# Performance work log

Measured on AMD Instinct MI355X. Metric: run time of the kernel, lower is better.

## Reference

```python
import jax, jax.numpy as jnp
import numpy as np

K = 128          # fixed max number of points per persistence diagram
BIG = 1e9        # sentinel for masked sort


def _extrema_masks(img):
    # 4-neighborhood local minima / maxima of a 2D image (boundary neighbors = +/-inf)
    p = jnp.pad(img, 1, constant_values=BIG)
    nmin = jnp.minimum(jnp.minimum(p[:-2, 1:-1], p[2:, 1:-1]),
                       jnp.minimum(p[1:-1, :-2], p[1:-1, 2:]))
    q = jnp.pad(img, 1, constant_values=-BIG)
    nmax = jnp.maximum(jnp.maximum(q[:-2, 1:-1], q[2:, 1:-1]),
                       jnp.maximum(q[1:-1, :-2], q[1:-1, 2:]))
    return img <= nmin, img >= nmax


def _diagrams(img):
    # Approximate persistence diagrams of the sublevel-set filtration of img.
    # H0: births at local minima (K smallest), deaths at local maxima (K smallest).
    # H1 (via superlevel duality approx): births at local maxima (K largest),
    #     deaths at local minima (K largest). Fixed cardinality K, invalid slots -> (0,0).
    is_min, is_max = _extrema_masks(img)
    flat = img.ravel()
    mn, mx = is_min.ravel(), is_max.ravel()

    b0 = jnp.sort(jnp.where(mn, flat, BIG))[:K]
    d0 = jnp.sort(jnp.where(mx, flat, BIG))[:K]
    v0 = (b0 < BIG / 2) & (d0 < BIG / 2)
    pd0 = jnp.where(v0[:, None], jnp.stack([b0, jnp.maximum(d0, b0)], -1), 0.0)

    b1 = -jnp.sort(jnp.where(mx, -flat, BIG))[:K]
    d1 = -jnp.sort(jnp.where(mn, -flat, BIG))[:K]
    v1 = (b1 > -BIG / 2) & (d1 > -BIG / 2)
    pd1 = jnp.where(v1[:, None], jnp.stack([b1, jnp.minimum(d1, b1)], -1), 0.0)
    return pd0, pd1


def _w2sq(pa, pb):
    # squared 2-Wasserstein with internal L2, matching points in sorted order
    # (sliced/order-matching approximation of the optimal diagram matching)
    return jnp.sum((pa - pb) ** 2)


def setup_inputs() -> dict:
    key = jax.random.key(0)
    k1, k2 = jax.random.split(key)
    inputs = jax.random.normal(k1, (256, 256, 256), dtype=jnp.float32)
    targets = jax.random.normal(k2, (256, 256, 256), dtype=jnp.float32)
    return {"inputs": inputs, "targets": targets}


def reference(inputs, targets):
    def per_sample(x, y):
        x0, x1 = _diagrams(x)
        y0, y1 = _diagrams(y)
        # wasserstein(pd0)^2 + wasserstein(pd1)^2, as in wasserstein_topological
        return _w2sq(x0, y0) + _w2sq(x1, y1)

    losses = jax.vmap(per_sample)(inputs, targets)  # [B]
    return jnp.mean(losses)  # reduction='mean'
```

## Files before the change

kernel.cpp:

```cpp
#include <hip/hip_runtime.h>
#include <stdint.h>


#define KPTS 128
#define BIGF 1.0e9f
#define IMG_W 256
#define NPIX (IMG_W * IMG_W)
#define NTH 1024
#define QITERS (NPIX / 4 / NTH)
#define SEGC 1024
#define LCAP (16 * SEGC)
#define HPAD 264

__device__ __forceinline__ uint32_t f2key(float f) {
    uint32_t u = __float_as_uint(f);
    return (u & 0x80000000u) ? ~u : (u | 0x80000000u);
}
__device__ __forceinline__ float key2f(uint32_t k) {
    uint32_t u = (k & 0x80000000u) ? (k ^ 0x80000000u) : ~k;
    return __uint_as_float(u);
}


template <bool WANTK>
__device__ __forceinline__ void stencilRow(const float* __restrict__ img, int row, int lane,
                                           bool mnf[4], bool mxf[4], uint32_t kk[4]) {
    const float* base = img + (size_t)row * IMG_W;
    float4 cur = *(const float4*)(base + lane * 4);
    bool hu = row > 0, hd = row < (IMG_W - 1);
    float4 up = cur, dn = cur;
    if (hu) up = *(const float4*)(base - IMG_W + lane * 4);
    if (hd) dn = *(const float4*)(base + IMG_W + lane * 4);
    float lft = __shfl_up(cur.w, 1);
    float rgt = __shfl_down(cur.x, 1);
    bool hl = (lane > 0), hr = (lane < 63);
    float cv[4] = {cur.x, cur.y, cur.z, cur.w};
    float uv[4] = {up.x, up.y, up.z, up.w};
    float dv[4] = {dn.x, dn.y, dn.z, dn.w};
    #pragma unroll
    for (int j = 0; j < 4; ++j) {
        float v = cv[j];
        bool el = (j > 0) || hl, er = (j < 3) || hr;
        float vl = (j > 0) ? cv[j - 1] : lft;
        float vr = (j < 3) ? cv[j + 1] : rgt;
        float nmn = fminf(fminf(el ? vl : BIGF, er ? vr : BIGF),
                          fminf(hu ? uv[j] : BIGF, hd ? dv[j] : BIGF));
        float nmx = fmaxf(fmaxf(el ? vl : -BIGF, er ? vr : -BIGF),
                          fmaxf(hu ? uv[j] : -BIGF, hd ? dv[j] : -BIGF));
        mnf[j] = (v <= nmn);
        mxf[j] = (v >= nmx);
        if (WANTK) kk[j] = f2key(cv[j]);
    }
}

__global__ __launch_bounds__(256) void topo_scan4_kernel(
        const float* __restrict__ X, const float* __restrict__ Y,
        uint32_t* __restrict__ gkeys, uint32_t* __restrict__ gcnt16, int B) {
    const int tid = threadIdx.x;
    const int lane = tid & 63;
    const int wv = tid >> 6;
    const int gw = blockIdx.x * 4 + wv;
    const int im = gw >> 4;
    const int seg = gw & 15;
    const int r0 = seg * 16;
    const float* img = ((im & 1) ? Y : X) + (size_t)(im >> 1) * NPIX;
    const float* base0 = img + (size_t)r0 * IMG_W + lane * 4;
    const unsigned long long ltm = (1ull << lane) - 1ull;

    uint32_t* dMin = gkeys + (size_t)(im * 2 + 0) * LCAP + seg * SEGC;
    uint32_t* dMax = gkeys + (size_t)(im * 2 + 1) * LCAP + seg * SEGC;
    uint32_t cMin = 0, cMax = 0;

    float4 cur  = *(const float4*)(base0);
    float4 prev = (r0 > 0) ? *(const float4*)(base0 - IMG_W) : cur;
    float4 next = *(const float4*)(base0 + IMG_W);

    for (int it = 0; it < 16; ++it) {
        const int row = r0 + it;
        const bool hu = row > 0, hd = row < (IMG_W - 1);
        float4 nxt2 = cur;
        if (it < 15 && row + 2 < IMG_W)
            nxt2 = *(const float4*)(base0 + (it + 2) * IMG_W);

        float lft = __shfl_up(cur.w, 1);
        float rgt = __shfl_down(cur.x, 1);
        bool hl = (lane > 0), hr = (lane < 63);
        float cv[4] = {cur.x, cur.y, cur.z, cur.w};
        float uv[4] = {prev.x, prev.y, prev.z, prev.w};
        float dv[4] = {next.x, next.y, next.z, next.w};
        bool mnf[4], mxf[4];
        uint32_t kk[4];
        #pragma unroll
        for (int j = 0; j < 4; ++j) {
            float v = cv[j];
            bool el = (j > 0) || hl, er = (j < 3) || hr;
            float vl = (j > 0) ? cv[j - 1] : lft;
            float vr = (j < 3) ? cv[j + 1] : rgt;
            float nmn = fminf(fminf(el ? vl : BIGF, er ? vr : BIGF),
                              fminf(hu ? uv[j] : BIGF, hd ? dv[j] : BIGF));
            float nmx = fmaxf(fmaxf(el ? vl : -BIGF, er ? vr : -BIGF),
                              fmaxf(hu ? uv[j] : -BIGF, hd ? dv[j] : -BIGF));
            mnf[j] = (v <= nmn);
            mxf[j] = (v >= nmx);
            kk[j] = f2key(v);
        }
        {
            unsigned long long m0 = __ballot(mnf[0]), m1 = __ballot(mnf[1]),
                               m2 = __ballot(mnf[2]), m3 = __ballot(mnf[3]);
            uint32_t c0 = (uint32_t)__popcll(m0), c1 = (uint32_t)__popcll(m1),
                     c2 = (uint32_t)__popcll(m2), c3 = (uint32_t)__popcll(m3);
            uint32_t o;
            if (mnf[0]) { o = cMin + (uint32_t)__popcll(m0 & ltm);                if (o < SEGC) dMin[o] = kk[0]; }
            if (mnf[1]) { o = cMin + c0 + (uint32_t)__popcll(m1 & ltm);           if (o < SEGC) dMin[o] = kk[1]; }
            if (mnf[2]) { o = cMin + c0 + c1 + (uint32_t)__popcll(m2 & ltm);      if (o < SEGC) dMin[o] = kk[2]; }
            if (mnf[3]) { o = cMin + c0 + c1 + c2 + (uint32_t)__popcll(m3 & ltm); if (o < SEGC) dMin[o] = kk[3]; }
            cMin += c0 + c1 + c2 + c3;
        }
        {
            unsigned long long m0 = __ballot(mxf[0]), m1 = __ballot(mxf[1]),
                               m2 = __ballot(mxf[2]), m3 = __ballot(mxf[3]);
            uint32_t c0 = (uint32_t)__popcll(m0), c1 = (uint32_t)__popcll(m1),
                     c2 = (uint32_t)__popcll(m2), c3 = (uint32_t)__popcll(m3);
            uint32_t o;
            if (mxf[0]) { o = cMax + (uint32_t)__popcll(m0 & ltm);                if (o < SEGC) dMax[o] = kk[0]; }
            if (mxf[1]) { o = cMax + c0 + (uint32_t)__popcll(m1 & ltm);           if (o < SEGC) dMax[o] = kk[1]; }
            if (mxf[2]) { o = cMax + c0 + c1 + (uint32_t)__popcll(m2 & ltm);      if (o < SEGC) dMax[o] = kk[2]; }
            if (mxf[3]) { o = cMax + c0 + c1 + c2 + (uint32_t)__popcll(m3 & ltm); if (o < SEGC) dMax[o] = kk[3]; }
            cMax += c0 + c1 + c2 + c3;
        }
        prev = cur; cur = next; next = nxt2;
    }
    if (lane == 0) {
        gcnt16[(im * 2 + 0) * 16 + seg] = (cMin < SEGC) ? cMin : SEGC;
        gcnt16[(im * 2 + 1) * 16 + seg] = (cMax < SEGC) ? cMax : SEGC;
    }
}

struct SMQ {
    uint32_t keys[LCAP];
    uint32_t h8[8 * HPAD];
    uint32_t pref[2], rank[2], ccnt[2];
    int      flagAll[2];
    float    buf[4][KPTS];
};

__device__ __forceinline__ void binSelP(const uint32_t* h, int ncop, int lane, uint32_t r,
                                        uint32_t& bsel, uint32_t& newr) {
    uint32_t b0 = 0, b1 = 0, b2 = 0, b3 = 0;
    for (int c = 0; c < ncop; ++c) {
        const uint32_t* hh = h + c * HPAD;
        b0 += hh[4 * lane];     b1 += hh[4 * lane + 1];
        b2 += hh[4 * lane + 2]; b3 += hh[4 * lane + 3];
    }
    uint32_t s4 = b0 + b1 + b2 + b3, cum = s4;
    #pragma unroll
    for (int d = 1; d < 64; d <<= 1) { uint32_t t = __shfl_up(cum, d); if (lane >= d) cum += t; }
    unsigned long long m = __ballot(cum > r);
    int L = (m == 0ull) ? 63 : __builtin_ctzll(m);
    uint32_t cumL = __shfl(cum, L), s4L = __shfl(s4, L);
    uint32_t a0 = __shfl(b0, L), a1 = __shfl(b1, L), a2 = __shfl(b2, L);
    uint32_t excl = cumL - s4L;
    if (excl + a0 > r)                { bsel = 4u * L;     newr = r - excl; }
    else if (excl + a0 + a1 > r)      { bsel = 4u * L + 1; newr = r - excl - a0; }
    else if (excl + a0 + a1 + a2 > r) { bsel = 4u * L + 2; newr = r - excl - a0 - a1; }
    else                              { bsel = 4u * L + 3; newr = r - excl - a0 - a1 - a2; }
}

__device__ __forceinline__ void waveSort128(float e[2], bool asc, int lane) {
    for (int size = 2; size <= 128; size <<= 1) {
        for (int stride = size >> 1; stride > 0; stride >>= 1) {
            if (stride == 64) {
                float a = e[0], b = e[1];
                e[0] = asc ? fminf(a, b) : fmaxf(a, b);
                e[1] = asc ? fmaxf(a, b) : fminf(a, b);
            } else {
                #pragma unroll
                for (int r = 0; r < 2; ++r) {
                    int i = r * 64 + lane;
                    float v = e[r];
                    float w = __shfl_xor(v, stride);
                    bool up = ((i & size) == 0) ? asc : !asc;
                    bool lower = (i & stride) == 0;
                    float mn = fminf(v, w), mx = fmaxf(v, w);
                    e[r] = (lower == up) ? mn : mx;
                }
            }
        }
    }
}

__global__ __launch_bounds__(NTH, 8) void topo_sel2_kernel(
        const uint32_t* __restrict__ gkeys, const uint32_t* __restrict__ gcnt16,
        float* __restrict__ diagOut, int B) {
    __shared__ SMQ sm;
    const int tid = threadIdx.x;
    const int lane = tid & 63;
    const int wv = tid >> 6;
    const int im = blockIdx.x;
    const int hc = lane & 7;

    for (int ph = 0; ph < 2; ++ph) {
        for (int i = tid; i < 8 * HPAD; i += NTH) sm.h8[i] = 0u;
        __syncthreads();
        const uint32_t* list = gkeys + (size_t)(im * 2 + ph) * LCAP;
        const uint32_t* cnts = gcnt16 + (im * 2 + ph) * 16;

        uint32_t cw = (lane < 16) ? cnts[lane] : 0;
        uint32_t inc = cw;
        #pragma unroll
        for (int d = 1; d < 16; d <<= 1) { uint32_t t = __shfl_up(inc, d); if (lane >= d) inc += t; }
        uint32_t C = __shfl(inc, 15);
        uint32_t myCnt = __shfl(cw, wv);
        uint32_t myOff = __shfl(inc, wv) - myCnt;

        for (uint32_t i = lane; i < myCnt; i += 64) {
            uint32_t k = list[wv * SEGC + i];
            sm.keys[myOff + i] = k;
            atomicAdd(&sm.h8[hc * HPAD + (k >> 24)], 1u);
        }
        __syncthreads();

        if (wv < 2) {
            bool low = (wv == 0);
            if (C < KPTS) {
                if (lane == 0) { sm.flagAll[wv] = 1; sm.pref[wv] = 0u; sm.rank[wv] = 0u; }
            } else {
                uint32_t bsel, nr;
                binSelP(sm.h8, 8, lane, low ? (KPTS - 1) : (C - KPTS), bsel, nr);
                if (lane == 0) { sm.flagAll[wv] = 0; sm.pref[wv] = bsel; sm.rank[wv] = nr; }
            }
        }
        __syncthreads();

        for (int lvl = 2; lvl >= 0; --lvl) {
            for (int i = tid; i < 2 * HPAD; i += NTH) sm.h8[i] = 0u;
            __syncthreads();
            int f0 = sm.flagAll[0], f1 = sm.flagAll[1];
            uint32_t p0 = sm.pref[0], p1 = sm.pref[1];
            const int sp = 8 * (lvl + 1), sb = 8 * lvl;
            for (uint32_t i = tid; i < C; i += NTH) {
                uint32_t k = sm.keys[i], hi = k >> sp, by = (k >> sb) & 255u;
                if (!f0 && hi == p0) atomicAdd(&sm.h8[by], 1u);
                if (!f1 && hi == p1) atomicAdd(&sm.h8[HPAD + by], 1u);
            }
            __syncthreads();
            if (wv < 2 && !sm.flagAll[wv]) {
                uint32_t bsel, nr;
                binSelP(&sm.h8[wv * HPAD], 1, lane, sm.rank[wv], bsel, nr);
                if (lane == 0) { sm.pref[wv] = (sm.pref[wv] << 8) | bsel; sm.rank[wv] = nr; }
            }
            __syncthreads();
        }

        if (tid < 2) sm.ccnt[tid] = 0u;
        __syncthreads();
        const int g0 = (ph == 0) ? 0 : 1;
        const int g1 = (ph == 0) ? 3 : 2;
        {
            int f0 = sm.flagAll[0], f1 = sm.flagAll[1];
            uint32_t t0 = sm.pref[0], t1 = sm.pref[1];
            for (uint32_t i = tid; i < C; i += NTH) {
                uint32_t k = sm.keys[i];
                if (f0 || k < t0) { uint32_t s = atomicAdd(&sm.ccnt[0], 1u); if (s < KPTS) sm.buf[g0][s] = key2f(k); }
                if (f1 || k > t1) { uint32_t s = atomicAdd(&sm.ccnt[1], 1u); if (s < KPTS) sm.buf[g1][s] = key2f(k); }
            }
        }
        __syncthreads();
        if (tid < 2 * KPTS) {
            int l = tid >> 7, i = tid & 127;
            int g = (l == 0) ? g0 : g1;
            if ((uint32_t)i >= sm.ccnt[l])
                sm.buf[g][i] = sm.flagAll[l] ? ((l == 0) ? BIGF : -BIGF) : key2f(sm.pref[l]);
        }
        __syncthreads();
    }

    if (wv < 4) {
        float e[2];
        e[0] = sm.buf[wv][lane];
        e[1] = sm.buf[wv][lane + 64];
        waveSort128(e, wv < 2, lane);
        diagOut[(size_t)im * 512 + wv * 128 + lane]      = e[0];
        diagOut[(size_t)im * 512 + wv * 128 + 64 + lane] = e[1];
    }
}

__global__ __launch_bounds__(128) void topo_loss_kernel(
        const float* __restrict__ diag, float* __restrict__ lossOut, int B) {
    const int s = blockIdx.x, i = threadIdx.x;
    const float* xw = diag + (size_t)(2 * s) * 512;
    const float* yw = xw + 512;
    const float H = 0.5f * BIGF;
    float b0x = xw[i], d0x = xw[128 + i], b1x = xw[256 + i], d1x = xw[384 + i];
    float b0y = yw[i], d0y = yw[128 + i], b1y = yw[256 + i], d1y = yw[384 + i];
    bool vx0 = (b0x < H) && (d0x < H);
    float px0b = vx0 ? b0x : 0.f, px0d = vx0 ? fmaxf(d0x, b0x) : 0.f;
    bool vy0 = (b0y < H) && (d0y < H);
    float py0b = vy0 ? b0y : 0.f, py0d = vy0 ? fmaxf(d0y, b0y) : 0.f;
    bool vx1 = (b1x > -H) && (d1x > -H);
    float px1b = vx1 ? b1x : 0.f, px1d = vx1 ? fminf(d1x, b1x) : 0.f;
    bool vy1 = (b1y > -H) && (d1y > -H);
    float py1b = vy1 ? b1y : 0.f, py1d = vy1 ? fminf(d1y, b1y) : 0.f;
    float e0 = px0b - py0b, e1 = px0d - py0d, e2 = px1b - py1b, e3 = px1d - py1d;
    float total = e0 * e0 + e1 * e1 + e2 * e2 + e3 * e3;
    for (int off = 32; off; off >>= 1) total += __shfl_down(total, off);
    __shared__ float lr[2];
    if ((i & 63) == 0) lr[i >> 6] = total;
    __syncthreads();
    if (i == 0) lossOut[s] = lr[0] + lr[1];
}

__global__ void topo_reduce_kernel(const float* __restrict__ ws, float* __restrict__ out, int B) {
    float v = 0.f;
    for (int i = threadIdx.x; i < B; i += 256) v += ws[i];
    __shared__ float r[4];
    for (int off = 32; off; off >>= 1) v += __shfl_down(v, off);
    if ((threadIdx.x & 63) == 0) r[threadIdx.x >> 6] = v;
    __syncthreads();
    if (threadIdx.x == 0) out[0] = (r[0] + r[1] + r[2] + r[3]) / (float)B;
}

struct SMP {
    uint32_t keys[LCAP];
    uint32_t h8[8][256];
    uint32_t cnt[2];
    uint32_t pref[2], rank[2], ccnt[2];
    int      flagAll[2];
    float    buf[4][KPTS];
};

__device__ __forceinline__ void binSelN(const uint32_t (*h)[256], int ncop, int lane, uint32_t r,
                                        uint32_t& bsel, uint32_t& newr) {
    uint32_t b0 = 0, b1 = 0, b2 = 0, b3 = 0;
    for (int c = 0; c < ncop; ++c) {
        b0 += h[c][4 * lane];     b1 += h[c][4 * lane + 1];
        b2 += h[c][4 * lane + 2]; b3 += h[c][4 * lane + 3];
    }
    uint32_t s4 = b0 + b1 + b2 + b3, cum = s4;
    #pragma unroll
    for (int d = 1; d < 64; d <<= 1) { uint32_t t = __shfl_up(cum, d); if (lane >= d) cum += t; }
    unsigned long long m = __ballot(cum > r);
    int L = (m == 0ull) ? 63 : __builtin_ctzll(m);
    uint32_t cumL = __shfl(cum, L), s4L = __shfl(s4, L);
    uint32_t a0 = __shfl(b0, L), a1 = __shfl(b1, L), a2 = __shfl(b2, L);
    uint32_t excl = cumL - s4L;
    if (excl + a0 > r)                { bsel = 4u * L;     newr = r - excl; }
    else if (excl + a0 + a1 > r)      { bsel = 4u * L + 1; newr = r - excl - a0; }
    else if (excl + a0 + a1 + a2 > r) { bsel = 4u * L + 2; newr = r - excl - a0 - a1; }
    else                              { bsel = 4u * L + 3; newr = r - excl - a0 - a1 - a2; }
}

__global__ __launch_bounds__(NTH, 8) void topo_pd3_kernel(
        const float* __restrict__ X, const float* __restrict__ Y,
        float* __restrict__ diagOut, int B) {
    __shared__ SMP sm;
    const int tid = threadIdx.x;
    const int lane = tid & 63;
    const int wv = tid >> 6;
    const int bid = blockIdx.x;
    const float* img = ((bid & 1) ? Y : X) + (size_t)(bid >> 1) * NPIX;
    const unsigned long long ltm = (1ull << lane) - 1ull;

    for (int ph = 0; ph < 2; ++ph) {
        for (int i = tid; i < 8 * 256; i += NTH) ((uint32_t*)sm.h8)[i] = 0u;
        if (tid == 0) sm.cnt[0] = 0u;
        __syncthreads();
        for (int it = 0; it < QITERS; ++it) {
            int q = it * NTH + tid;
            int p = q * 4;
            int row = p >> 8;
            bool mnf[4], mxf[4]; uint32_t kk[4];
            stencilRow<true>(img, row, lane, mnf, mxf, kk);
            bool e0 = (ph == 0) ? mnf[0] : mxf[0], e1 = (ph == 0) ? mnf[1] : mxf[1];
            bool e2 = (ph == 0) ? mnf[2] : mxf[2], e3 = (ph == 0) ? mnf[3] : mxf[3];
            unsigned long long m0 = __ballot(e0), m1 = __ballot(e1),
                               m2 = __ballot(e2), m3 = __ballot(e3);
            uint32_t c0 = (uint32_t)__popcll(m0), c1 = (uint32_t)__popcll(m1),
                     c2 = (uint32_t)__popcll(m2), c3 = (uint32_t)__popcll(m3);
            uint32_t base = 0;
            if (lane == 0) base = atomicAdd(&sm.cnt[0], c0 + c1 + c2 + c3);
            base = __shfl(base, 0);
            uint32_t o;
            if (e0) { o = base + (uint32_t)__popcll(m0 & ltm);                sm.keys[o < LCAP ? o : LCAP - 1] = kk[0]; atomicAdd(&sm.h8[wv >> 1][kk[0] >> 24], 1u); }
            if (e1) { o = base + c0 + (uint32_t)__popcll(m1 & ltm);           sm.keys[o < LCAP ? o : LCAP - 1] = kk[1]; atomicAdd(&sm.h8[wv >> 1][kk[1] >> 24], 1u); }
            if (e2) { o = base + c0 + c1 + (uint32_t)__popcll(m2 & ltm);      sm.keys[o < LCAP ? o : LCAP - 1] = kk[2]; atomicAdd(&sm.h8[wv >> 1][kk[2] >> 24], 1u); }
            if (e3) { o = base + c0 + c1 + c2 + (uint32_t)__popcll(m3 & ltm); sm.keys[o < LCAP ? o : LCAP - 1] = kk[3]; atomicAdd(&sm.h8[wv >> 1][kk[3] >> 24], 1u); }
        }
        __syncthreads();
        uint32_t C = sm.cnt[0]; if (C > LCAP) C = LCAP;

        if (wv < 2) {
            bool low = (wv == 0);
            if (C < KPTS) {
                if (lane == 0) { sm.flagAll[wv] = 1; sm.pref[wv] = 0u; sm.rank[wv] = 0u; }
            } else {
                uint32_t bsel, nr;
                binSelN(sm.h8, 8, lane, low ? (KPTS - 1) : (C - KPTS), bsel, nr);
                if (lane == 0) { sm.flagAll[wv] = 0; sm.pref[wv] = bsel; sm.rank[wv] = nr; }
            }
        }
        __syncthreads();

        for (int lvl = 2; lvl >= 0; --lvl) {
            for (int i = tid; i < 2 * 256; i += NTH) ((uint32_t*)sm.h8)[i] = 0u;
            __syncthreads();
            int f0 = sm.flagAll[0], f1 = sm.flagAll[1];
            uint32_t p0 = sm.pref[0], p1 = sm.pref[1];
            const int sp = 8 * (lvl + 1), sb = 8 * lvl;
            for (uint32_t i = tid; i < C; i += NTH) {
                uint32_t k = sm.keys[i], hi = k >> sp, by = (k >> sb) & 255u;
                if (!f0 && hi == p0) atomicAdd(&sm.h8[0][by], 1u);
                if (!f1 && hi == p1) atomicAdd(&sm.h8[1][by], 1u);
            }
            __syncthreads();
            if (wv < 2 && !sm.flagAll[wv]) {
                uint32_t bsel, nr;
                binSelN((const uint32_t(*)[256])&sm.h8[wv], 1, lane, sm.rank[wv], bsel, nr);
                if (lane == 0) { sm.pref[wv] = (sm.pref[wv] << 8) | bsel; sm.rank[wv] = nr; }
            }
            __syncthreads();
        }

        if (tid < 2) sm.ccnt[tid] = 0u;
        __syncthreads();
        const int g0 = (ph == 0) ? 0 : 1;
        const int g1 = (ph == 0) ? 3 : 2;
        {
            int f0 = sm.flagAll[0], f1 = sm.flagAll[1];
            uint32_t t0 = sm.pref[0], t1 = sm.pref[1];
            for (uint32_t i = tid; i < C; i += NTH) {
                uint32_t k = sm.keys[i];
                if (f0 || k < t0) { uint32_t s = atomicAdd(&sm.ccnt[0], 1u); if (s < KPTS) sm.buf[g0][s] = key2f(k); }
                if (f1 || k > t1) { uint32_t s = atomicAdd(&sm.ccnt[1], 1u); if (s < KPTS) sm.buf[g1][s] = key2f(k); }
            }
        }
        __syncthreads();
        if (tid < 2 * KPTS) {
            int l = tid >> 7, i = tid & 127;
            int g = (l == 0) ? g0 : g1;
            if ((uint32_t)i >= sm.ccnt[l])
                sm.buf[g][i] = sm.flagAll[l] ? ((l == 0) ? BIGF : -BIGF) : key2f(sm.pref[l]);
        }
        __syncthreads();
    }

    if (wv < 4) {
        float e[2];
        e[0] = sm.buf[wv][lane];
        e[1] = sm.buf[wv][lane + 64];
        waveSort128(e, wv < 2, lane);
        diagOut[(size_t)bid * 512 + wv * 128 + lane]      = e[0];
        diagOut[(size_t)bid * 512 + wv * 128 + 64 + lane] = e[1];
    }
}

extern "C" void kernel_launch(void* const* d_in, const int* in_sizes, int n_in,
                              void* d_out, int out_size, void* d_ws, size_t ws_size,
                              hipStream_t stream) {
    const float* X = (const float*)d_in[0];
    const float* Y = (const float*)d_in[1];
    float* out = (float*)d_out;
    const int B = in_sizes[0] / NPIX;

    size_t diagSz = (size_t)2 * B * 512 * sizeof(float);
    size_t lossSz = (size_t)B * sizeof(float);
    size_t cntSz  = (size_t)2 * B * 2 * 16 * sizeof(uint32_t);
    size_t keysSz = (size_t)2 * B * 2 * LCAP * sizeof(uint32_t);

    if (ws_size >= diagSz + lossSz + cntSz + keysSz) {
        float* diag = (float*)d_ws;
        float* lossbuf = (float*)((char*)d_ws + diagSz);
        uint32_t* gcnt16 = (uint32_t*)((char*)d_ws + diagSz + lossSz);
        uint32_t* gkeys = (uint32_t*)((char*)d_ws + diagSz + lossSz + cntSz);
        topo_scan4_kernel<<<8 * B, 256, 0, stream>>>(X, Y, gkeys, gcnt16, B);
        topo_sel2_kernel<<<2 * B, NTH, 0, stream>>>(gkeys, gcnt16, diag, B);
        topo_loss_kernel<<<B, 128, 0, stream>>>(diag, lossbuf, B);
        topo_reduce_kernel<<<1, 256, 0, stream>>>(lossbuf, out, B);
    } else if (ws_size >= diagSz + lossSz) {
        float* diag = (float*)d_ws;
        float* lossbuf = (float*)((char*)d_ws + diagSz);
        topo_pd3_kernel<<<2 * B, NTH, 0, stream>>>(X, Y, diag, B);
        topo_loss_kernel<<<B, 128, 0, stream>>>(diag, lossbuf, B);
        topo_reduce_kernel<<<1, 256, 0, stream>>>(lossbuf, out, B);
    } else {
        topo_pd3_kernel<<<2 * B, NTH, 0, stream>>>(X, Y, (float*)d_ws, B);
    }
}
```

Measured before the change: 90.32 us.

## Split scan waves by extremum type and fuse selection with loss

The scan kernel now launches twice as many waves, and each wave handles only minima or only maxima for its row segment. That halves the per-wave ballot and store work and raises parallelism, but every image row is read twice. The selection kernel now processes both the X and Y images of a sample in one block and computes the per-sample loss in place, removing the separate loss kernel and the diagram round trip through global memory. The catch is half as many selection blocks (B instead of 2B), each doing serial work on two images.

```diff
diff --git a/kernel.cpp b/kernel.cpp
--- a/kernel.cpp
+++ b/kernel.cpp
@@ -21,6 +21,268 @@
     return __uint_as_float(u);
 }
 
+
+template <bool ISMAX>
+__device__ __forceinline__ uint32_t scanSegT(const float* __restrict__ base0, int r0, int lane,
+                                             unsigned long long ltm, uint32_t* __restrict__ dst) {
+    uint32_t cnt = 0;
+    float4 cur  = *(const float4*)(base0);
+    float4 prev = (r0 > 0) ? *(const float4*)(base0 - IMG_W) : cur;
+    float4 next = *(const float4*)(base0 + IMG_W);
+    for (int it = 0; it < 16; ++it) {
+        const int row = r0 + it;
+        const bool hu = row > 0, hd = row < (IMG_W - 1);
+        float4 nxt2 = cur;
+        if (it < 15 && row + 2 < IMG_W)
+            nxt2 = *(const float4*)(base0 + (it + 2) * IMG_W);
+        float lft = __shfl_up(cur.w, 1);
+        float rgt = __shfl_down(cur.x, 1);
+        bool hl = (lane > 0), hr = (lane < 63);
+        float cv[4] = {cur.x, cur.y, cur.z, cur.w};
+        float uv[4] = {prev.x, prev.y, prev.z, prev.w};
+        float dv[4] = {next.x, next.y, next.z, next.w};
+        bool fl[4]; uint32_t kk[4];
+        #pragma unroll
+        for (int j = 0; j < 4; ++j) {
+            float v = cv[j];
+            bool el = (j > 0) || hl, er = (j < 3) || hr;
+            float vl = (j > 0) ? cv[j - 1] : lft;
+            float vr = (j < 3) ? cv[j + 1] : rgt;
+            if (ISMAX) {
+                float nmx = fmaxf(fmaxf(el ? vl : -BIGF, er ? vr : -BIGF),
+                                  fmaxf(hu ? uv[j] : -BIGF, hd ? dv[j] : -BIGF));
+                fl[j] = (v >= nmx);
+            } else {
+                float nmn = fminf(fminf(el ? vl : BIGF, er ? vr : BIGF),
+                                  fminf(hu ? uv[j] : BIGF, hd ? dv[j] : BIGF));
+                fl[j] = (v <= nmn);
+            }
+            kk[j] = f2key(v);
+        }
+        unsigned long long m0 = __ballot(fl[0]), m1 = __ballot(fl[1]),
+                           m2 = __ballot(fl[2]), m3 = __ballot(fl[3]);
+        uint32_t c0 = (uint32_t)__popcll(m0), c1 = (uint32_t)__popcll(m1),
+                 c2 = (uint32_t)__popcll(m2), c3 = (uint32_t)__popcll(m3);
+        uint32_t o;
+        if (fl[0]) { o = cnt + (uint32_t)__popcll(m0 & ltm);                if (o < SEGC) dst[o] = kk[0]; }
+        if (fl[1]) { o = cnt + c0 + (uint32_t)__popcll(m1 & ltm);           if (o < SEGC) dst[o] = kk[1]; }
+        if (fl[2]) { o = cnt + c0 + c1 + (uint32_t)__popcll(m2 & ltm);      if (o < SEGC) dst[o] = kk[2]; }
+        if (fl[3]) { o = cnt + c0 + c1 + c2 + (uint32_t)__popcll(m3 & ltm); if (o < SEGC) dst[o] = kk[3]; }
+        cnt += c0 + c1 + c2 + c3;
+        prev = cur; cur = next; next = nxt2;
+    }
+    return cnt;
+}
+
+__global__ __launch_bounds__(256) void topo_scan6_kernel(
+        const float* __restrict__ X, const float* __restrict__ Y,
+        uint32_t* __restrict__ gkeys, uint32_t* __restrict__ gcnt16, int B) {
+    const int tid = threadIdx.x;
+    const int lane = tid & 63;
+    const int wv = tid >> 6;
+    const int gw = blockIdx.x * 4 + wv;
+    const int im = gw >> 5;
+    const int type = (gw >> 4) & 1;
+    const int seg = gw & 15;
+    const int r0 = seg * 16;
+    const float* img = ((im & 1) ? Y : X) + (size_t)(im >> 1) * NPIX;
+    const float* base0 = img + (size_t)r0 * IMG_W + lane * 4;
+    const unsigned long long ltm = (1ull << lane) - 1ull;
+
+    uint32_t* dst = gkeys + (size_t)(im * 2 + type) * LCAP + seg * SEGC;
+    uint32_t cnt = type ? scanSegT<true>(base0, r0, lane, ltm, dst)
+                        : scanSegT<false>(base0, r0, lane, ltm, dst);
+    if (lane == 0)
+        gcnt16[(im * 2 + type) * 16 + seg] = (cnt < SEGC) ? cnt : SEGC;
+}
+
+struct SMR {
+    uint32_t keys[LCAP];
+    uint32_t h8[8 * HPAD];
+    uint32_t pref[2], rank[2], ccnt[2];
+    int      flagAll[2];
+    float    buf[4][KPTS];
+    float    res[2][4][KPTS];
+    float    lred[2];
+};
+
+__device__ __forceinline__ void binSelP(const uint32_t* h, int ncop, int lane, uint32_t r,
+                                        uint32_t& bsel, uint32_t& newr) {
+    uint32_t b0 = 0, b1 = 0, b2 = 0, b3 = 0;
+    for (int c = 0; c < ncop; ++c) {
+        const uint32_t* hh = h + c * HPAD;
+        b0 += hh[4 * lane];     b1 += hh[4 * lane + 1];
+        b2 += hh[4 * lane + 2]; b3 += hh[4 * lane + 3];
+    }
+    uint32_t s4 = b0 + b1 + b2 + b3, cum = s4;
+    #pragma unroll
+    for (int d = 1; d < 64; d <<= 1) { uint32_t t = __shfl_up(cum, d); if (lane >= d) cum += t; }
+    unsigned long long m = __ballot(cum > r);
+    int L = (m == 0ull) ? 63 : __builtin_ctzll(m);
+    uint32_t cumL = __shfl(cum, L), s4L = __shfl(s4, L);
+    uint32_t a0 = __shfl(b0, L), a1 = __shfl(b1, L), a2 = __shfl(b2, L);
+    uint32_t excl = cumL - s4L;
+    if (excl + a0 > r)                { bsel = 4u * L;     newr = r - excl; }
+    else if (excl + a0 + a1 > r)      { bsel = 4u * L + 1; newr = r - excl - a0; }
+    else if (excl + a0 + a1 + a2 > r) { bsel = 4u * L + 2; newr = r - excl - a0 - a1; }
+    else                              { bsel = 4u * L + 3; newr = r - excl - a0 - a1 - a2; }
+}
+
+__device__ __forceinline__ void waveSort128(float e[2], bool asc, int lane) {
+    for (int size = 2; size <= 128; size <<= 1) {
+        for (int stride = size >> 1; stride > 0; stride >>= 1) {
+            if (stride == 64) {
+                float a = e[0], b = e[1];
+                e[0] = asc ? fminf(a, b) : fmaxf(a, b);
+                e[1] = asc ? fmaxf(a, b) : fminf(a, b);
+            } else {
+                #pragma unroll
+                for (int r = 0; r < 2; ++r) {
+                    int i = r * 64 + lane;
+                    float v = e[r];
+                    float w = __shfl_xor(v, stride);
+                    bool up = ((i & size) == 0) ? asc : !asc;
+                    bool lower = (i & stride) == 0;
+                    float mn = fminf(v, w), mx = fmaxf(v, w);
+                    e[r] = (lower == up) ? mn : mx;
+                }
+            }
+        }
+    }
+}
+
+__global__ __launch_bounds__(NTH, 8) void topo_sel3_kernel(
+        const uint32_t* __restrict__ gkeys, const uint32_t* __restrict__ gcnt16,
+        float* __restrict__ lossOut, int B) {
+    __shared__ SMR sm;
+    const int tid = threadIdx.x;
+    const int lane = tid & 63;
+    const int wv = tid >> 6;
+    const int s = blockIdx.x;
+    const int hc = lane & 7;
+
+    for (int half = 0; half < 2; ++half) {
+        const int imgIdx = 2 * s + half;
+        for (int ph = 0; ph < 2; ++ph) {
+            for (int i = tid; i < 8 * HPAD; i += NTH) sm.h8[i] = 0u;
+            __syncthreads();
+            const uint32_t* list = gkeys + (size_t)(imgIdx * 2 + ph) * LCAP;
+            const uint32_t* cnts = gcnt16 + (imgIdx * 2 + ph) * 16;
+
+            uint32_t cw = (lane < 16) ? cnts[lane] : 0;
+            uint32_t inc = cw;
+            #pragma unroll
+            for (int d = 1; d < 16; d <<= 1) { uint32_t t = __shfl_up(inc, d); if (lane >= d) inc += t; }
+            uint32_t C = __shfl(inc, 15);
+            uint32_t myCnt = __shfl(cw, wv);
+            uint32_t myOff = __shfl(inc, wv) - myCnt;
+
+            for (uint32_t i = lane; i < myCnt; i += 64) {
+                uint32_t k = list[wv * SEGC + i];
+                sm.keys[myOff + i] = k;
+                atomicAdd(&sm.h8[hc * HPAD + (k >> 24)], 1u);
+            }
+            __syncthreads();
+
+            if (wv < 2) {
+                bool low = (wv == 0);
+                if (C < KPTS) {
+                    if (lane == 0) { sm.flagAll[wv] = 1; sm.pref[wv] = 0u; sm.rank[wv] = 0u; }
+                } else {
+                    uint32_t bsel, nr;
+                    binSelP(sm.h8, 8, lane, low ? (KPTS - 1) : (C - KPTS), bsel, nr);
+                    if (lane == 0) { sm.flagAll[wv] = 0; sm.pref[wv] = bsel; sm.rank[wv] = nr; }
+                }
+            }
+            __syncthreads();
+
+            for (int lvl = 2; lvl >= 0; --lvl) {
+                for (int i = tid; i < 2 * HPAD; i += NTH) sm.h8[i] = 0u;
+                __syncthreads();
+                int f0 = sm.flagAll[0], f1 = sm.flagAll[1];
+                uint32_t p0 = sm.pref[0], p1 = sm.pref[1];
+                const int sp = 8 * (lvl + 1), sb = 8 * lvl;
+                for (uint32_t i = tid; i < C; i += NTH) {
+                    uint32_t k = sm.keys[i], hi = k >> sp, by = (k >> sb) & 255u;
+                    if (!f0 && hi == p0) atomicAdd(&sm.h8[by], 1u);
+                    if (!f1 && hi == p1) atomicAdd(&sm.h8[HPAD + by], 1u);
+                }
+                __syncthreads();
+                if (wv < 2 && !sm.flagAll[wv]) {
+                    uint32_t bsel, nr;
+                    binSelP(&sm.h8[wv * HPAD], 1, lane, sm.rank[wv], bsel, nr);
+                    if (lane == 0) { sm.pref[wv] = (sm.pref[wv] << 8) | bsel; sm.rank[wv] = nr; }
+                }
+                __syncthreads();
+            }
+
+            if (tid < 2) sm.ccnt[tid] = 0u;
+            __syncthreads();
+            const int g0 = (ph == 0) ? 0 : 1;
+            const int g1 = (ph == 0) ? 3 : 2;
+            {
+                int f0 = sm.flagAll[0], f1 = sm.flagAll[1];
+                uint32_t t0 = sm.pref[0], t1 = sm.pref[1];
+                for (uint32_t i = tid; i < C; i += NTH) {
+                    uint32_t k = sm.keys[i];
+                    if (f0 || k < t0) { uint32_t q = atomicAdd(&sm.ccnt[0], 1u); if (q < KPTS) sm.buf[g0][q] = key2f(k); }
+                    if (f1 || k > t1) { uint32_t q = atomicAdd(&sm.ccnt[1], 1u); if (q < KPTS) sm.buf[g1][q] = key2f(k); }
+                }
+            }
+            __syncthreads();
+            if (tid < 2 * KPTS) {
+                int l = tid >> 7, i = tid & 127;
+                int g = (l == 0) ? g0 : g1;
+                if ((uint32_t)i >= sm.ccnt[l])
+                    sm.buf[g][i] = sm.flagAll[l] ? ((l == 0) ? BIGF : -BIGF) : key2f(sm.pref[l]);
+            }
+            __syncthreads();
+        }
+
+        if (wv < 4) {
+            float e[2];
+            e[0] = sm.buf[wv][lane];
+            e[1] = sm.buf[wv][lane + 64];
+            waveSort128(e, wv < 2, lane);
+            sm.res[half][wv][lane]      = e[0];
+            sm.res[half][wv][lane + 64] = e[1];
+        }
+        __syncthreads();
+    }
+
+    float total = 0.f;
+    if (tid < KPTS) {
+        int i = tid;
+        const float H = 0.5f * BIGF;
+        float b0x = sm.res[0][0][i], d0x = sm.res[0][1][i], b1x = sm.res[0][2][i], d1x = sm.res[0][3][i];
+        float b0y = sm.res[1][0][i], d0y = sm.res[1][1][i], b1y = sm.res[1][2][i], d1y = sm.res[1][3][i];
+        bool vx0 = (b0x < H) && (d0x < H);
+        float px0b = vx0 ? b0x : 0.f, px0d = vx0 ? fmaxf(d0x, b0x) : 0.f;
+        bool vy0 = (b0y < H) && (d0y < H);
+        float py0b = vy0 ? b0y : 0.f, py0d = vy0 ? fmaxf(d0y, b0y) : 0.f;
+        bool vx1 = (b1x > -H) && (d1x > -H);
+        float px1b = vx1 ? b1x : 0.f, px1d = vx1 ? fminf(d1x, b1x) : 0.f;
+        bool vy1 = (b1y > -H) && (d1y > -H);
+        float py1b = vy1 ? b1y : 0.f, py1d = vy1 ? fminf(d1y, b1y) : 0.f;
+        float e0 = px0b - py0b, e1 = px0d - py0d, e2 = px1b - py1b, e3 = px1d - py1d;
+        total = e0 * e0 + e1 * e1 + e2 * e2 + e3 * e3;
+    }
+    for (int off = 32; off; off >>= 1) total += __shfl_down(total, off);
+    if (tid == 0)  sm.lred[0] = total;
+    if (tid == 64) sm.lred[1] = total;
+    __syncthreads();
+    if (tid == 0) lossOut[s] = sm.lred[0] + sm.lred[1];
+}
+
+__global__ void topo_reduce_kernel(const float* __restrict__ ws, float* __restrict__ out, int B) {
+    float v = 0.f;
+    for (int i = threadIdx.x; i < B; i += 256) v += ws[i];
+    __shared__ float r[4];
+    for (int off = 32; off; off >>= 1) v += __shfl_down(v, off);
+    if ((threadIdx.x & 63) == 0) r[threadIdx.x >> 6] = v;
+    __syncthreads();
+    if (threadIdx.x == 0) out[0] = (r[0] + r[1] + r[2] + r[3]) / (float)B;
+}
 
 template <bool WANTK>
 __device__ __forceinline__ void stencilRow(const float* __restrict__ img, int row, int lane,
@@ -53,104 +315,21 @@
     }
 }
 
-__global__ __launch_bounds__(256) void topo_scan4_kernel(
-        const float* __restrict__ X, const float* __restrict__ Y,
-        uint32_t* __restrict__ gkeys, uint32_t* __restrict__ gcnt16, int B) {
-    const int tid = threadIdx.x;
-    const int lane = tid & 63;
-    const int wv = tid >> 6;
-    const int gw = blockIdx.x * 4 + wv;
-    const int im = gw >> 4;
-    const int seg = gw & 15;
-    const int r0 = seg * 16;
-    const float* img = ((im & 1) ? Y : X) + (size_t)(im >> 1) * NPIX;
-    const float* base0 = img + (size_t)r0 * IMG_W + lane * 4;
-    const unsigned long long ltm = (1ull << lane) - 1ull;
-
-    uint32_t* dMin = gkeys + (size_t)(im * 2 + 0) * LCAP + seg * SEGC;
-    uint32_t* dMax = gkeys + (size_t)(im * 2 + 1) * LCAP + seg * SEGC;
-    uint32_t cMin = 0, cMax = 0;
-
-    float4 cur  = *(const float4*)(base0);
-    float4 prev = (r0 > 0) ? *(const float4*)(base0 - IMG_W) : cur;
-    float4 next = *(const float4*)(base0 + IMG_W);
-
-    for (int it = 0; it < 16; ++it) {
-        const int row = r0 + it;
-        const bool hu = row > 0, hd = row < (IMG_W - 1);
-        float4 nxt2 = cur;
-        if (it < 15 && row + 2 < IMG_W)
-            nxt2 = *(const float4*)(base0 + (it + 2) * IMG_W);
-
-        float lft = __shfl_up(cur.w, 1);
-        float rgt = __shfl_down(cur.x, 1);
-        bool hl = (lane > 0), hr = (lane < 63);
-        float cv[4] = {cur.x, cur.y, cur.z, cur.w};
-        float uv[4] = {prev.x, prev.y, prev.z, prev.w};
-        float dv[4] = {next.x, next.y, next.z, next.w};
-        bool mnf[4], mxf[4];
-        uint32_t kk[4];
-        #pragma unroll
-        for (int j = 0; j < 4; ++j) {
-            float v = cv[j];
-            bool el = (j > 0) || hl, er = (j < 3) || hr;
-            float vl = (j > 0) ? cv[j - 1] : lft;
-            float vr = (j < 3) ? cv[j + 1] : rgt;
-            float nmn = fminf(fminf(el ? vl : BIGF, er ? vr : BIGF),
-                              fminf(hu ? uv[j] : BIGF, hd ? dv[j] : BIGF));
-            float nmx = fmaxf(fmaxf(el ? vl : -BIGF, er ? vr : -BIGF),
-                              fmaxf(hu ? uv[j] : -BIGF, hd ? dv[j] : -BIGF));
-            mnf[j] = (v <= nmn);
-            mxf[j] = (v >= nmx);
-            kk[j] = f2key(v);
-        }
-        {
-            unsigned long long m0 = __ballot(mnf[0]), m1 = __ballot(mnf[1]),
-                               m2 = __ballot(mnf[2]), m3 = __ballot(mnf[3]);
-            uint32_t c0 = (uint32_t)__popcll(m0), c1 = (uint32_t)__popcll(m1),
-                     c2 = (uint32_t)__popcll(m2), c3 = (uint32_t)__popcll(m3);
-            uint32_t o;
-            if (mnf[0]) { o = cMin + (uint32_t)__popcll(m0 & ltm);                if (o < SEGC) dMin[o] = kk[0]; }
-            if (mnf[1]) { o = cMin + c0 + (uint32_t)__popcll(m1 & ltm);           if (o < SEGC) dMin[o] = kk[1]; }
-            if (mnf[2]) { o = cMin + c0 + c1 + (uint32_t)__popcll(m2 & ltm);      if (o < SEGC) dMin[o] = kk[2]; }
-            if (mnf[3]) { o = cMin + c0 + c1 + c2 + (uint32_t)__popcll(m3 & ltm); if (o < SEGC) dMin[o] = kk[3]; }
-            cMin += c0 + c1 + c2 + c3;
-        }
-        {
-            unsigned long long m0 = __ballot(mxf[0]), m1 = __ballot(mxf[1]),
-                               m2 = __ballot(mxf[2]), m3 = __ballot(mxf[3]);
-            uint32_t c0 = (uint32_t)__popcll(m0), c1 = (uint32_t)__popcll(m1),
-                     c2 = (uint32_t)__popcll(m2), c3 = (uint32_t)__popcll(m3);
-            uint32_t o;
-            if (mxf[0]) { o = cMax + (uint32_t)__popcll(m0 & ltm);                if (o < SEGC) dMax[o] = kk[0]; }
-            if (mxf[1]) { o = cMax + c0 + (uint32_t)__popcll(m1 & ltm);           if (o < SEGC) dMax[o] = kk[1]; }
-            if (mxf[2]) { o = cMax + c0 + c1 + (uint32_t)__popcll(m2 & ltm);      if (o < SEGC) dMax[o] = kk[2]; }
-            if (mxf[3]) { o = cMax + c0 + c1 + c2 + (uint32_t)__popcll(m3 & ltm); if (o < SEGC) dMax[o] = kk[3]; }
-            cMax += c0 + c1 + c2 + c3;
-        }
-        prev = cur; cur = next; next = nxt2;
-    }
-    if (lane == 0) {
-        gcnt16[(im * 2 + 0) * 16 + seg] = (cMin < SEGC) ? cMin : SEGC;
-        gcnt16[(im * 2 + 1) * 16 + seg] = (cMax < SEGC) ? cMax : SEGC;
-    }
-}
-
-struct SMQ {
+struct SMP {
     uint32_t keys[LCAP];
-    uint32_t h8[8 * HPAD];
+    uint32_t h8[8][256];
+    uint32_t cnt[2];
     uint32_t pref[2], rank[2], ccnt[2];
     int      flagAll[2];
     float    buf[4][KPTS];
 };
 
-__device__ __forceinline__ void binSelP(const uint32_t* h, int ncop, int lane, uint32_t r,
+__device__ __forceinline__ void binSelN(const uint32_t (*h)[256], int ncop, int lane, uint32_t r,
                                         uint32_t& bsel, uint32_t& newr) {
     uint32_t b0 = 0, b1 = 0, b2 = 0, b3 = 0;
     for (int c = 0; c < ncop; ++c) {
-        const uint32_t* hh = h + c * HPAD;
-        b0 += hh[4 * lane];     b1 += hh[4 * lane + 1];
-        b2 += hh[4 * lane + 2]; b3 += hh[4 * lane + 3];
+        b0 += h[c][4 * lane];     b1 += h[c][4 * lane + 1];
+        b2 += h[c][4 * lane + 2]; b3 += h[c][4 * lane + 3];
     }
     uint32_t s4 = b0 + b1 + b2 + b3, cum = s4;
     #pragma unroll
@@ -166,59 +345,44 @@
     else                              { bsel = 4u * L + 3; newr = r - excl - a0 - a1 - a2; }
 }
 
-__device__ __forceinline__ void waveSort128(float e[2], bool asc, int lane) {
-    for (int size = 2; size <= 128; size <<= 1) {
-        for (int stride = size >> 1; stride > 0; stride >>= 1) {
-            if (stride == 64) {
-                float a = e[0], b = e[1];
-                e[0] = asc ? fminf(a, b) : fmaxf(a, b);
-                e[1] = asc ? fmaxf(a, b) : fminf(a, b);
-            } else {
-                #pragma unroll
-                for (int r = 0; r < 2; ++r) {
-                    int i = r * 64 + lane;
-                    float v = e[r];
-                    float w = __shfl_xor(v, stride);
-                    bool up = ((i & size) == 0) ? asc : !asc;
-                    bool lower = (i & stride) == 0;
-                    float mn = fminf(v, w), mx = fmaxf(v, w);
-                    e[r] = (lower == up) ? mn : mx;
-                }
-            }
-        }
-    }
-}
-
-__global__ __launch_bounds__(NTH, 8) void topo_sel2_kernel(
-        const uint32_t* __restrict__ gkeys, const uint32_t* __restrict__ gcnt16,
+__global__ __launch_bounds__(NTH, 8) void topo_pd3_kernel(
+        const float* __restrict__ X, const float* __restrict__ Y,
         float* __restrict__ diagOut, int B) {
-    __shared__ SMQ sm;
+    __shared__ SMP sm;
     const int tid = threadIdx.x;
     const int lane = tid & 63;
     const int wv = tid >> 6;
-    const int im = blockIdx.x;
-    const int hc = lane & 7;
+    const int bid = blockIdx.x;
+    const float* img = ((bid & 1) ? Y : X) + (size_t)(bid >> 1) * NPIX;
+    const unsigned long long ltm = (1ull << lane) - 1ull;
 
     for (int ph = 0; ph < 2; ++ph) {
-        for (int i = tid; i < 8 * HPAD; i += NTH) sm.h8[i] = 0u;
-        __syncthreads();
-        const uint32_t* list = gkeys + (size_t)(im * 2 + ph) * LCAP;
-        const uint32_t* cnts = gcnt16 + (im * 2 + ph) * 16;
-
-        uint32_t cw = (lane < 16) ? cnts[lane] : 0;
-        uint32_t inc = cw;
-        #pragma unroll
-        for (int d = 1; d < 16; d <<= 1) { uint32_t t = __shfl_up(inc, d); if (lane >= d) inc += t; }
-        uint32_t C = __shfl(inc, 15);
-        uint32_t myCnt = __shfl(cw, wv);
-        uint32_t myOff = __shfl(inc, wv) - myCnt;
-
-        for (uint32_t i = lane; i < myCnt; i += 64) {
-            uint32_t k = list[wv * SEGC + i];
-            sm.keys[myOff + i] = k;
-            atomicAdd(&sm.h8[hc * HPAD + (k >> 24)], 1u);
-        }
-        __syncthreads();
+        for (int i = tid; i < 8 * 256; i += NTH) ((uint32_t*)sm.h8)[i] = 0u;
+        if (tid == 0) sm.cnt[0] = 0u;
+        __syncthreads();
+        for (int it = 0; it < QITERS; ++it) {
+            int q = it * NTH + tid;
+            int p = q * 4;
+            int row = p >> 8;
+            bool mnf[4], mxf[4]; uint32_t kk[4];
+            stencilRow<true>(img, row, lane, mnf, mxf, kk);
+            bool e0 = (ph == 0) ? mnf[0] : mxf[0], e1 = (ph == 0) ? mnf[1] : mxf[1];
+            bool e2 = (ph == 0) ? mnf[2] : mxf[2], e3 = (ph == 0) ? mnf[3] : mxf[3];
+            unsigned long long m0 = __ballot(e0), m1 = __ballot(e1),
+                               m2 = __ballot(e2), m3 = __ballot(e3);
+            uint32_t c0 = (uint32_t)__popcll(m0), c1 = (uint32_t)__popcll(m1),
+                     c2 = (uint32_t)__popcll(m2), c3 = (uint32_t)__popcll(m3);
+            uint32_t base = 0;
+            if (lane == 0) base = atomicAdd(&sm.cnt[0], c0 + c1 + c2 + c3);
+            base = __shfl(base, 0);
+            uint32_t o;
+            if (e0) { o = base + (uint32_t)__popcll(m0 & ltm);                sm.keys[o < LCAP ? o : LCAP - 1] = kk[0]; atomicAdd(&sm.h8[wv >> 1][kk[0] >> 24], 1u); }
+            if (e1) { o = base + c0 + (uint32_t)__popcll(m1 & ltm);           sm.keys[o < LCAP ? o : LCAP - 1] = kk[1]; atomicAdd(&sm.h8[wv >> 1][kk[1] >> 24], 1u); }
+            if (e2) { o = base + c0 + c1 + (uint32_t)__popcll(m2 & ltm);      sm.keys[o < LCAP ? o : LCAP - 1] = kk[2]; atomicAdd(&sm.h8[wv >> 1][kk[2] >> 24], 1u); }
+            if (e3) { o = base + c0 + c1 + c2 + (uint32_t)__popcll(m3 & ltm); sm.keys[o < LCAP ? o : LCAP - 1] = kk[3]; atomicAdd(&sm.h8[wv >> 1][kk[3] >> 24], 1u); }
+        }
+        __syncthreads();
+        uint32_t C = sm.cnt[0]; if (C > LCAP) C = LCAP;
 
         if (wv < 2) {
             bool low = (wv == 0);
@@ -226,27 +390,27 @@
                 if (lane == 0) { sm.flagAll[wv] = 1; sm.pref[wv] = 0u; sm.rank[wv] = 0u; }
             } else {
                 uint32_t bsel, nr;
-                binSelP(sm.h8, 8, lane, low ? (KPTS - 1) : (C - KPTS), bsel, nr);
+                binSelN(sm.h8, 8, lane, low ? (KPTS - 1) : (C - KPTS), bsel, nr);
                 if (lane == 0) { sm.flagAll[wv] = 0; sm.pref[wv] = bsel; sm.rank[wv] = nr; }
             }
         }
         __syncthreads();
 
         for (int lvl = 2; lvl >= 0; --lvl) {
-            for (int i = tid; i < 2 * HPAD; i += NTH) sm.h8[i] = 0u;
+            for (int i = tid; i < 2 * 256; i += NTH) ((uint32_t*)sm.h8)[i] = 0u;
             __syncthreads();
             int f0 = sm.flagAll[0], f1 = sm.flagAll[1];
             uint32_t p0 = sm.pref[0], p1 = sm.pref[1];
             const int sp = 8 * (lvl + 1), sb = 8 * lvl;
             for (uint32_t i = tid; i < C; i += NTH) {
                 uint32_t k = sm.keys[i], hi = k >> sp, by = (k >> sb) & 255u;
-                if (!f0 && hi == p0) atomicAdd(&sm.h8[by], 1u);
-                if (!f1 && hi == p1) atomicAdd(&sm.h8[HPAD + by], 1u);
+                if (!f0 && hi == p0) atomicAdd(&sm.h8[0][by], 1u);
+                if (!f1 && hi == p1) atomicAdd(&sm.h8[1][by], 1u);
             }
             __syncthreads();
             if (wv < 2 && !sm.flagAll[wv]) {
                 uint32_t bsel, nr;
-                binSelP(&sm.h8[wv * HPAD], 1, lane, sm.rank[wv], bsel, nr);
+                binSelN((const uint32_t(*)[256])&sm.h8[wv], 1, lane, sm.rank[wv], bsel, nr);
                 if (lane == 0) { sm.pref[wv] = (sm.pref[wv] << 8) | bsel; sm.rank[wv] = nr; }
             }
             __syncthreads();
@@ -261,8 +425,8 @@
             uint32_t t0 = sm.pref[0], t1 = sm.pref[1];
             for (uint32_t i = tid; i < C; i += NTH) {
                 uint32_t k = sm.keys[i];
-                if (f0 || k < t0) { uint32_t s = atomicAdd(&sm.ccnt[0], 1u); if (s < KPTS) sm.buf[g0][s] = key2f(k); }
-                if (f1 || k > t1) { uint32_t s = atomicAdd(&sm.ccnt[1], 1u); if (s < KPTS) sm.buf[g1][s] = key2f(k); }
+                if (f0 || k < t0) { uint32_t q = atomicAdd(&sm.ccnt[0], 1u); if (q < KPTS) sm.buf[g0][q] = key2f(k); }
+                if (f1 || k > t1) { uint32_t q = atomicAdd(&sm.ccnt[1], 1u); if (q < KPTS) sm.buf[g1][q] = key2f(k); }
             }
         }
         __syncthreads();
@@ -280,8 +444,8 @@
         e[0] = sm.buf[wv][lane];
         e[1] = sm.buf[wv][lane + 64];
         waveSort128(e, wv < 2, lane);
-        diagOut[(size_t)im * 512 + wv * 128 + lane]      = e[0];
-        diagOut[(size_t)im * 512 + wv * 128 + 64 + lane] = e[1];
+        diagOut[(size_t)bid * 512 + wv * 128 + lane]      = e[0];
+        diagOut[(size_t)bid * 512 + wv * 128 + 64 + lane] = e[1];
     }
 }
 
@@ -310,150 +474,6 @@
     if (i == 0) lossOut[s] = lr[0] + lr[1];
 }
 
-__global__ void topo_reduce_kernel(const float* __restrict__ ws, float* __restrict__ out, int B) {
-    float v = 0.f;
-    for (int i = threadIdx.x; i < B; i += 256) v += ws[i];
-    __shared__ float r[4];
-    for (int off = 32; off; off >>= 1) v += __shfl_down(v, off);
-    if ((threadIdx.x & 63) == 0) r[threadIdx.x >> 6] = v;
-    __syncthreads();
-    if (threadIdx.x == 0) out[0] = (r[0] + r[1] + r[2] + r[3]) / (float)B;
-}
-
-struct SMP {
-    uint32_t keys[LCAP];
-    uint32_t h8[8][256];
-    uint32_t cnt[2];
-    uint32_t pref[2], rank[2], ccnt[2];
-    int      flagAll[2];
-    float    buf[4][KPTS];
-};
-
-__device__ __forceinline__ void binSelN(const uint32_t (*h)[256], int ncop, int lane, uint32_t r,
-                                        uint32_t& bsel, uint32_t& newr) {
-    uint32_t b0 = 0, b1 = 0, b2 = 0, b3 = 0;
-    for (int c = 0; c < ncop; ++c) {
-        b0 += h[c][4 * lane];     b1 += h[c][4 * lane + 1];
-        b2 += h[c][4 * lane + 2]; b3 += h[c][4 * lane + 3];
-    }
-    uint32_t s4 = b0 + b1 + b2 + b3, cum = s4;
-    #pragma unroll
-    for (int d = 1; d < 64; d <<= 1) { uint32_t t = __shfl_up(cum, d); if (lane >= d) cum += t; }
-    unsigned long long m = __ballot(cum > r);
-    int L = (m == 0ull) ? 63 : __builtin_ctzll(m);
-    uint32_t cumL = __shfl(cum, L), s4L = __shfl(s4, L);
-    uint32_t a0 = __shfl(b0, L), a1 = __shfl(b1, L), a2 = __shfl(b2, L);
-    uint32_t excl = cumL - s4L;
-    if (excl + a0 > r)                { bsel = 4u * L;     newr = r - excl; }
-    else if (excl + a0 + a1 > r)      { bsel = 4u * L + 1; newr = r - excl - a0; }
-    else if (excl + a0 + a1 + a2 > r) { bsel = 4u * L + 2; newr = r - excl - a0 - a1; }
-    else                              { bsel = 4u * L + 3; newr = r - excl - a0 - a1 - a2; }
-}
-
-__global__ __launch_bounds__(NTH, 8) void topo_pd3_kernel(
-        const float* __restrict__ X, const float* __restrict__ Y,
-        float* __restrict__ diagOut, int B) {
-    __shared__ SMP sm;
-    const int tid = threadIdx.x;
-    const int lane = tid & 63;
-    const int wv = tid >> 6;
-    const int bid = blockIdx.x;
-    const float* img = ((bid & 1) ? Y : X) + (size_t)(bid >> 1) * NPIX;
-    const unsigned long long ltm = (1ull << lane) - 1ull;
-
-    for (int ph = 0; ph < 2; ++ph) {
-        for (int i = tid; i < 8 * 256; i += NTH) ((uint32_t*)sm.h8)[i] = 0u;
-        if (tid == 0) sm.cnt[0] = 0u;
-        __syncthreads();
-        for (int it = 0; it < QITERS; ++it) {
-            int q = it * NTH + tid;
-            int p = q * 4;
-            int row = p >> 8;
-            bool mnf[4], mxf[4]; uint32_t kk[4];
-            stencilRow<true>(img, row, lane, mnf, mxf, kk);
-            bool e0 = (ph == 0) ? mnf[0] : mxf[0], e1 = (ph == 0) ? mnf[1] : mxf[1];
-            bool e2 = (ph == 0) ? mnf[2] : mxf[2], e3 = (ph == 0) ? mnf[3] : mxf[3];
-            unsigned long long m0 = __ballot(e0), m1 = __ballot(e1),
-                               m2 = __ballot(e2), m3 = __ballot(e3);
-            uint32_t c0 = (uint32_t)__popcll(m0), c1 = (uint32_t)__popcll(m1),
-                     c2 = (uint32_t)__popcll(m2), c3 = (uint32_t)__popcll(m3);
-            uint32_t base = 0;
-            if (lane == 0) base = atomicAdd(&sm.cnt[0], c0 + c1 + c2 + c3);
-            base = __shfl(base, 0);
-            uint32_t o;
-            if (e0) { o = base + (uint32_t)__popcll(m0 & ltm);                sm.keys[o < LCAP ? o : LCAP - 1] = kk[0]; atomicAdd(&sm.h8[wv >> 1][kk[0] >> 24], 1u); }
-            if (e1) { o = base + c0 + (uint32_t)__popcll(m1 & ltm);           sm.keys[o < LCAP ? o : LCAP - 1] = kk[1]; atomicAdd(&sm.h8[wv >> 1][kk[1] >> 24], 1u); }
-            if (e2) { o = base + c0 + c1 + (uint32_t)__popcll(m2 & ltm);      sm.keys[o < LCAP ? o : LCAP - 1] = kk[2]; atomicAdd(&sm.h8[wv >> 1][kk[2] >> 24], 1u); }
-            if (e3) { o = base + c0 + c1 + c2 + (uint32_t)__popcll(m3 & ltm); sm.keys[o < LCAP ? o : LCAP - 1] = kk[3]; atomicAdd(&sm.h8[wv >> 1][kk[3] >> 24], 1u); }
-        }
-        __syncthreads();
-        uint32_t C = sm.cnt[0]; if (C > LCAP) C = LCAP;
-
-        if (wv < 2) {
-            bool low = (wv == 0);
-            if (C < KPTS) {
-                if (lane == 0) { sm.flagAll[wv] = 1; sm.pref[wv] = 0u; sm.rank[wv] = 0u; }
-            } else {
-                uint32_t bsel, nr;
-                binSelN(sm.h8, 8, lane, low ? (KPTS - 1) : (C - KPTS), bsel, nr);
-                if (lane == 0) { sm.flagAll[wv] = 0; sm.pref[wv] = bsel; sm.rank[wv] = nr; }
-            }
-        }
-        __syncthreads();
-
-        for (int lvl = 2; lvl >= 0; --lvl) {
-            for (int i = tid; i < 2 * 256; i += NTH) ((uint32_t*)sm.h8)[i] = 0u;
-            __syncthreads();
-            int f0 = sm.flagAll[0], f1 = sm.flagAll[1];
-            uint32_t p0 = sm.pref[0], p1 = sm.pref[1];
-            const int sp = 8 * (lvl + 1), sb = 8 * lvl;
-            for (uint32_t i = tid; i < C; i += NTH) {
-                uint32_t k = sm.keys[i], hi = k >> sp, by = (k >> sb) & 255u;
-                if (!f0 && hi == p0) atomicAdd(&sm.h8[0][by], 1u);
-                if (!f1 && hi == p1) atomicAdd(&sm.h8[1][by], 1u);
-            }
-            __syncthreads();
-            if (wv < 2 && !sm.flagAll[wv]) {
-                uint32_t bsel, nr;
-                binSelN((const uint32_t(*)[256])&sm.h8[wv], 1, lane, sm.rank[wv], bsel, nr);
-                if (lane == 0) { sm.pref[wv] = (sm.pref[wv] << 8) | bsel; sm.rank[wv] = nr; }
-            }
-            __syncthreads();
-        }
-
-        if (tid < 2) sm.ccnt[tid] = 0u;
-        __syncthreads();
-        const int g0 = (ph == 0) ? 0 : 1;
-        const int g1 = (ph == 0) ? 3 : 2;
-        {
-            int f0 = sm.flagAll[0], f1 = sm.flagAll[1];
-            uint32_t t0 = sm.pref[0], t1 = sm.pref[1];
-            for (uint32_t i = tid; i < C; i += NTH) {
-                uint32_t k = sm.keys[i];
-                if (f0 || k < t0) { uint32_t s = atomicAdd(&sm.ccnt[0], 1u); if (s < KPTS) sm.buf[g0][s] = key2f(k); }
-                if (f1 || k > t1) { uint32_t s = atomicAdd(&sm.ccnt[1], 1u); if (s < KPTS) sm.buf[g1][s] = key2f(k); }
-            }
-        }
-        __syncthreads();
-        if (tid < 2 * KPTS) {
-            int l = tid >> 7, i = tid & 127;
-            int g = (l == 0) ? g0 : g1;
-            if ((uint32_t)i >= sm.ccnt[l])
-                sm.buf[g][i] = sm.flagAll[l] ? ((l == 0) ? BIGF : -BIGF) : key2f(sm.pref[l]);
-        }
-        __syncthreads();
-    }
-
-    if (wv < 4) {
-        float e[2];
-        e[0] = sm.buf[wv][lane];
-        e[1] = sm.buf[wv][lane + 64];
-        waveSort128(e, wv < 2, lane);
-        diagOut[(size_t)bid * 512 + wv * 128 + lane]      = e[0];
-        diagOut[(size_t)bid * 512 + wv * 128 + 64 + lane] = e[1];
-    }
-}
-
 extern "C" void kernel_launch(void* const* d_in, const int* in_sizes, int n_in,
                               void* d_out, int out_size, void* d_ws, size_t ws_size,
                               hipStream_t stream) {
@@ -462,19 +482,17 @@
     float* out = (float*)d_out;
     const int B = in_sizes[0] / NPIX;
 
-    size_t diagSz = (size_t)2 * B * 512 * sizeof(float);
     size_t lossSz = (size_t)B * sizeof(float);
     size_t cntSz  = (size_t)2 * B * 2 * 16 * sizeof(uint32_t);
     size_t keysSz = (size_t)2 * B * 2 * LCAP * sizeof(uint32_t);
-
-    if (ws_size >= diagSz + lossSz + cntSz + keysSz) {
-        float* diag = (float*)d_ws;
-        float* lossbuf = (float*)((char*)d_ws + diagSz);
-        uint32_t* gcnt16 = (uint32_t*)((char*)d_ws + diagSz + lossSz);
-        uint32_t* gkeys = (uint32_t*)((char*)d_ws + diagSz + lossSz + cntSz);
-        topo_scan4_kernel<<<8 * B, 256, 0, stream>>>(X, Y, gkeys, gcnt16, B);
-        topo_sel2_kernel<<<2 * B, NTH, 0, stream>>>(gkeys, gcnt16, diag, B);
-        topo_loss_kernel<<<B, 128, 0, stream>>>(diag, lossbuf, B);
+    size_t diagSz = (size_t)2 * B * 512 * sizeof(float);
+
+    if (ws_size >= lossSz + cntSz + keysSz) {
+        float* lossbuf = (float*)d_ws;
+        uint32_t* gcnt16 = (uint32_t*)((char*)d_ws + lossSz);
+        uint32_t* gkeys = (uint32_t*)((char*)d_ws + lossSz + cntSz);
+        topo_scan6_kernel<<<16 * B, 256, 0, stream>>>(X, Y, gkeys, gcnt16, B);
+        topo_sel3_kernel<<<B, NTH, 0, stream>>>(gkeys, gcnt16, lossbuf, B);
         topo_reduce_kernel<<<1, 256, 0, stream>>>(lossbuf, out, B);
     } else if (ws_size >= diagSz + lossSz) {
         float* diag = (float*)d_ws;
```

Result: slower. 124.7 us (+38.1%).
